# Kernel optimization log

Hardware: AMD Instinct MI355X
Metric: run time of the kernel (lower is better)

Reference implementation:

```python
import jax, jax.numpy as jnp
import numpy as np

B, N, DIM, H, DH, MLP, DEPTH = 32, 256, 384, 6, 64, 1536, 12
INNER = H * DH
LN_EPS = 1e-5
LS_INIT = 0.1  # LayerScale init_eps for depth <= 18


def setup_inputs() -> dict:
    key = jax.random.key(0)
    ks = jax.random.split(key, 10)
    f = lambda k, shape, s=0.02: jax.random.normal(k, shape, jnp.float32) * s
    return {
        "x": jax.random.normal(ks[0], (B, N, DIM), jnp.float32),
        "ln1_g": jnp.ones((DEPTH, DIM), jnp.float32),
        "ln1_b": jnp.zeros((DEPTH, DIM), jnp.float32),
        "wq": f(ks[1], (DEPTH, DIM, INNER)),
        "wkv": f(ks[2], (DEPTH, DIM, 2 * INNER)),
        "scale": jnp.full((DEPTH, H), DH ** -0.5, jnp.float32),  # learned per-head scale
        "mix_pre": f(ks[3], (DEPTH, H, H), 1.0),   # torch.randn init
        "mix_post": f(ks[4], (DEPTH, H, H), 1.0),
        "wo": f(ks[5], (DEPTH, INNER, DIM)),
        "bo": jnp.zeros((DEPTH, DIM), jnp.float32),
        "ls1": jnp.full((DEPTH, DIM), LS_INIT, jnp.float32),
        "ln2_g": jnp.ones((DEPTH, DIM), jnp.float32),
        "ln2_b": jnp.zeros((DEPTH, DIM), jnp.float32),
        "w1": f(ks[6], (DEPTH, DIM, MLP)),
        "b1": jnp.zeros((DEPTH, MLP), jnp.float32),
        "w2": f(ks[7], (DEPTH, MLP, DIM)),
        "b2": jnp.zeros((DEPTH, DIM), jnp.float32),
        "ls2": jnp.full((DEPTH, DIM), LS_INIT, jnp.float32),
    }


def _layernorm(x, g, b):
    mu = jnp.mean(x, axis=-1, keepdims=True)
    var = jnp.mean(jnp.square(x - mu), axis=-1, keepdims=True)
    return (x - mu) * jax.lax.rsqrt(var + LN_EPS) * g + b


def reference(x, ln1_g, ln1_b, wq, wkv, scale, mix_pre, mix_post, wo, bo, ls1,
              ln2_g, ln2_b, w1, b1, w2, b2, ls2):
    diag = jnp.eye(N, dtype=bool)  # self-attention diagonal mask

    def block(x, p):
        (g1, bb1, wq_, wkv_, sc, mp, mq, wo_, bo_, l1,
         g2, bb2, w1_, b1_, w2_, b2_, l2) = p
        # --- talking-heads attention (PreNorm + LayerScale + residual) ---
        y = _layernorm(x, g1, bb1)
        q = (y @ wq_).reshape(B, N, H, DH).transpose(0, 2, 1, 3)       # b h n d
        kv = y @ wkv_
        k, v = jnp.split(kv, 2, axis=-1)
        k = k.reshape(B, N, H, DH).transpose(0, 2, 1, 3)
        v = v.reshape(B, N, H, DH).transpose(0, 2, 1, 3)
        dots = jnp.einsum('bhid,bhjd->bhij', q, k) * sc[None, :, None, None]
        dots = jnp.einsum('bhij,hg->bgij', dots, mp)                   # pre-softmax head mix
        dots = jnp.where(diag, -jnp.inf, dots)                         # mask self positions
        attn = jax.nn.softmax(dots, axis=-1)
        attn = jnp.einsum('bhij,hg->bgij', attn, mq)                   # post-softmax head mix
        o = jnp.einsum('bhij,bhjd->bhid', attn, v)
        o = o.transpose(0, 2, 1, 3).reshape(B, N, INNER) @ wo_ + bo_
        x = o * l1 + x
        # --- FFN (PreNorm + LayerScale + residual) ---
        y2 = _layernorm(x, g2, bb2)
        h = jax.nn.gelu(y2 @ w1_ + b1_, approximate=False)
        x = (h @ w2_ + b2_) * l2 + x
        return x, None

    params = (ln1_g, ln1_b, wq, wkv, scale, mix_pre, mix_post, wo, bo, ls1,
              ln2_g, ln2_b, w1, b1, w2, b2, ls2)
    x, _ = jax.lax.scan(block, x, params)
    return x
```

## Files before the change

### kernel.cpp

```cpp
#include <hip/hip_runtime.h>
#include <hip/hip_bf16.h>
#include <math.h>

#define B_ 32
#define N_ 256
#define DIM_ 384
#define H_ 6
#define DH_ 64
#define INNER_ 384
#define MLP_ 1536
#define DEPTH_ 12
#define T_ (B_ * N_)

typedef __bf16 bf16x8 __attribute__((ext_vector_type(8)));
typedef __bf16 bf16x4 __attribute__((ext_vector_type(4)));
typedef float f32x4 __attribute__((ext_vector_type(4)));

typedef const __attribute__((address_space(1))) void* gas_ptr;
typedef __attribute__((address_space(3))) void* las_ptr;

#define WQKV_OFF 0
#define WO_OFF   (1152 * 384)
#define W1_OFF   (WO_OFF + 384 * 384)
#define W2_OFF   (W1_OFF + 1536 * 384)
#define WBUF_ELEMS (W2_OFF + 384 * 1536)

__global__ __launch_bounds__(256) void convert_w_all(
    const float* __restrict__ wq0, const float* __restrict__ wkv0,
    const float* __restrict__ wo0, const float* __restrict__ w10,
    const float* __restrict__ w20, __bf16* __restrict__ wbuf0)
{
    __shared__ float til[64][65];
    int t = blockIdx.x;
    int l = t / 432; t -= l * 432;
    const float* wq  = wq0  + (size_t)l * DIM_ * INNER_;
    const float* wkv = wkv0 + (size_t)l * DIM_ * 2 * INNER_;
    const float* wo  = wo0  + (size_t)l * INNER_ * DIM_;
    const float* w1  = w10  + (size_t)l * DIM_ * MLP_;
    const float* w2  = w20  + (size_t)l * MLP_ * DIM_;
    __bf16* wbuf = wbuf0 + (size_t)l * WBUF_ELEMS;

    int lane = threadIdx.x & 63, seg = threadIdx.x >> 6;
    const float* src; __bf16* dst;
    int Ns, sc, dK, dR, k0;
    if (t < 108) {
        int nt = t / 6, kt = t % 6;
        int n0 = nt * 64; k0 = kt * 64;
        dst = wbuf + WQKV_OFF; dK = 384; dR = n0;
        if (n0 < 384) { src = wq;  Ns = 384; sc = n0; }
        else          { src = wkv; Ns = 768; sc = n0 - 384; }
    } else if (t < 144) {
        int u = t - 108; int nt = u / 6, kt = u % 6;
        src = wo; Ns = 384; sc = nt * 64;
        dst = wbuf + WO_OFF; dK = 384; dR = nt * 64; k0 = kt * 64;
    } else if (t < 288) {
        int u = t - 144; int nt = u / 6, kt = u % 6;
        src = w1; Ns = 1536; sc = nt * 64;
        dst = wbuf + W1_OFF; dK = 384; dR = nt * 64; k0 = kt * 64;
    } else {
        int u = t - 288; int nt = u / 24, kt = u % 24;
        src = w2; Ns = 384; sc = nt * 64;
        dst = wbuf + W2_OFF; dK = 1536; dR = nt * 64; k0 = kt * 64;
    }
    #pragma unroll
    for (int r = 0; r < 16; ++r) {
        int i = seg * 16 + r;
        til[i][lane] = src[(size_t)(k0 + i) * Ns + sc + lane];
    }
    __syncthreads();
    #pragma unroll
    for (int r = 0; r < 16; ++r) {
        int i = seg * 16 + r;
        dst[(size_t)(dR + i) * dK + k0 + lane] = (__bf16)til[lane][i];
    }
}

__global__ __launch_bounds__(256) void ln1w(
    const float* __restrict__ x, const float* __restrict__ g,
    const float* __restrict__ b, __bf16* __restrict__ y)
{
    size_t row = blockIdx.x * 4 + (threadIdx.x >> 6);
    int lane = threadIdx.x & 63;
    const float* xr = x + row * DIM_;
    float v[6];
    #pragma unroll
    for (int s = 0; s < 6; ++s) v[s] = xr[lane + 64 * s];
    float sum = 0.f;
    #pragma unroll
    for (int s = 0; s < 6; ++s) sum += v[s];
    #pragma unroll
    for (int o = 32; o > 0; o >>= 1) sum += __shfl_xor(sum, o);
    float mu = sum * (1.0f / DIM_);
    float var = 0.f;
    #pragma unroll
    for (int s = 0; s < 6; ++s) { float d = v[s] - mu; var += d * d; }
    #pragma unroll
    for (int o = 32; o > 0; o >>= 1) var += __shfl_xor(var, o);
    float rs = rsqrtf(var * (1.0f / DIM_) + 1e-5f);
    __bf16* yr = y + row * DIM_;
    #pragma unroll
    for (int s = 0; s < 6; ++s) {
        int e = lane + 64 * s;
        yr[e] = (__bf16)((v[s] - mu) * rs * g[e] + b[e]);
    }
}

template<int MODE, int K, int BM, int BN, int BK, int NT>
__global__ __launch_bounds__(256) void gemmt(
    const __bf16* __restrict__ A, const __bf16* __restrict__ Bt,
    const float* __restrict__ bias, const float* __restrict__ ls,
    float* __restrict__ xf, __bf16* __restrict__ out,
    __bf16* __restrict__ oq, __bf16* __restrict__ ok, __bf16* __restrict__ ov,
    int Nn)
{
    constexpr int WM = BM / 32, WN = BN / 32;
    constexpr int KS = BK / 32;
    constexpr int MT = T_ / BM;
    constexpr int nIter = K / BK;
    constexpr bool SWZ = (BK == 64);
    constexpr int RPI = 512 / BK;
    constexpr int CL  = BK / 8;
    constexpr int LPT = BM / (4 * RPI) + BN / (4 * RPI);
    static_assert(LPT == 4, "vmcnt literals assume 4 loads per tile per wave");
    static_assert(nIter >= 2, "prologue stages 2 tiles");

    __shared__ __align__(16) __bf16 sA[3][BM * BK];
    __shared__ __align__(16) __bf16 sB[3][BN * BK];

    int id = blockIdx.x;
    constexpr int nxg = (MT * NT) / 8;
    int wg = (id & 7) * nxg + (id >> 3);
    int bm = (wg / NT) * BM;
    int bn = (wg % NT) * BN;
    int tid = threadIdx.x;
    int lane = tid & 63, wid = tid >> 6;
    int wm = (wid & 1) * (BM / 2), wn = (wid >> 1) * (BN / 2);
    int fm = lane & 15, fq = lane >> 4;

    f32x4 acc[WM][WN] = {};

    int lr = lane / CL, lc = lane % CL;
    int lcs = SWZ ? (lc ^ lr) : lc;
    const __bf16* aBase = A + (size_t)(bm + wid * RPI + lr) * K + lcs * 8;
    const __bf16* bBase = Bt + (size_t)(bn + wid * RPI + lr) * K + lcs * 8;

    auto stage = [&](int buf, int kk) {
        #pragma unroll
        for (int qI = 0; qI < BM / (4 * RPI); ++qI)
            __builtin_amdgcn_global_load_lds(
                (gas_ptr)(aBase + (size_t)(qI * 4 * RPI) * K + kk),
                (las_ptr)&sA[buf][qI * 2048 + wid * 512], 16, 0, 0);
        #pragma unroll
        for (int qI = 0; qI < BN / (4 * RPI); ++qI)
            __builtin_amdgcn_global_load_lds(
                (gas_ptr)(bBase + (size_t)(qI * 4 * RPI) * K + kk),
                (las_ptr)&sB[buf][qI * 2048 + wid * 512], 16, 0, 0);
    };

    stage(0, 0);
    stage(1, BK);

    #pragma unroll
    for (int i = 0; i < nIter; ++i) {
        int cur = i % 3;
        if (i + 1 < nIter)
            asm volatile("s_waitcnt vmcnt(4)" ::: "memory");
        else
            asm volatile("s_waitcnt vmcnt(0)" ::: "memory");
        __builtin_amdgcn_s_barrier();
        __builtin_amdgcn_sched_barrier(0);
        if (i + 2 < nIter)
            stage((i + 2) % 3, (i + 2) * BK);

        bf16x8 af[KS][WM], bfr[KS][WN];
        #pragma unroll
        for (int ks = 0; ks < KS; ++ks) {
            #pragma unroll
            for (int ii = 0; ii < WM; ++ii) {
                int row = wm + ii * 16 + fm;
                int c = SWZ ? (((ks * 4 + fq) ^ (row & 7)) * 8) : (ks * 32 + fq * 8);
                af[ks][ii] = *(const bf16x8*)&sA[cur][row * BK + c];
            }
            #pragma unroll
            for (int jj = 0; jj < WN; ++jj) {
                int row = wn + jj * 16 + fm;
                int c = SWZ ? (((ks * 4 + fq) ^ (row & 7)) * 8) : (ks * 32 + fq * 8);
                bfr[ks][jj] = *(const bf16x8*)&sB[cur][row * BK + c];
            }
        }
        #pragma unroll
        for (int ks = 0; ks < KS; ++ks)
            #pragma unroll
            for (int ii = 0; ii < WM; ++ii)
                #pragma unroll
                for (int jj = 0; jj < WN; ++jj)
                    acc[ii][jj] = __builtin_amdgcn_mfma_f32_16x16x32_bf16(
                        af[ks][ii], bfr[ks][jj], acc[ii][jj], 0, 0, 0);
    }

    #pragma unroll
    for (int jj = 0; jj < WN; ++jj) {
        int col = bn + wn + jj * 16 + fm;
        float bv = (MODE != 0) ? bias[col] : 0.0f;
        float lv = (MODE == 2) ? ls[col] : 0.0f;
        #pragma unroll
        for (int ii = 0; ii < WM; ++ii) {
            #pragma unroll
            for (int r = 0; r < 4; ++r) {
                int row = bm + wm + ii * 16 + fq * 4 + r;
                float v = acc[ii][jj][r];
                if (MODE == 0) {
                    if (col < 384)      oq[(size_t)row * 384 + col] = (__bf16)v;
                    else if (col < 768) ok[(size_t)row * 384 + col - 384] = (__bf16)v;
                    else {
                        int bb = row >> 8, tj = row & 255;
                        ov[((size_t)bb * 384 + (col - 768)) * 256 + tj] = (__bf16)v;
                    }
                } else if (MODE == 1) {
                    v += bv;
                    v = 0.5f * v * (1.0f + erff(v * 0.70710678118f));
                    out[(size_t)row * Nn + col] = (__bf16)v;
                } else {
                    size_t idx = (size_t)row * Nn + col;
                    xf[idx] = (v + bv) * lv + xf[idx];
                }
            }
        }
    }
}

#define PAD_S 264

__global__ __launch_bounds__(384) void attn_mfma(
    const __bf16* __restrict__ q, const __bf16* __restrict__ kb,
    const __bf16* __restrict__ vT, const float* __restrict__ scale,
    const float* __restrict__ mp, const float* __restrict__ mq,
    __bf16* __restrict__ o)
{
    __shared__ __bf16 sbuf[96][PAD_S];

    int id = blockIdx.x;
    int b = (id & 7) + ((id >> 3) & 3) * 8;
    int i0 = (id >> 5) * 16;
    int tid = threadIdx.x;
    int lane = tid & 63, wid = tid >> 6;
    int fm = lane & 15, fq = lane >> 4;

    int h = wid;
    bf16x8 qf[2];
    #pragma unroll
    for (int ks = 0; ks < 2; ++ks)
        qf[ks] = *(const bf16x8*)&q[(size_t)(b * 256 + i0 + fm) * 384 + h * 64 + ks * 32 + fq * 8];
    #pragma unroll 4
    for (int jt = 0; jt < 16; ++jt) {
        f32x4 a = {};
        #pragma unroll
        for (int ks = 0; ks < 2; ++ks) {
            bf16x8 bfr = *(const bf16x8*)&kb[(size_t)(b * 256 + jt * 16 + fm) * 384 + h * 64 + ks * 32 + fq * 8];
            a = __builtin_amdgcn_mfma_f32_16x16x32_bf16(qf[ks], bfr, a, 0, 0, 0);
        }
        #pragma unroll
        for (int r = 0; r < 4; ++r)
            sbuf[h * 16 + fq * 4 + r][jt * 16 + fm] = (__bf16)a[r];
    }

    float mps[36], mqs[36];
    #pragma unroll
    for (int t = 0; t < 36; ++t) { mps[t] = mp[t] * scale[t / 6]; mqs[t] = mq[t]; }

    __syncthreads();

    for (int i = wid; i < 16; i += 6) {
        float sv[6][4];
        #pragma unroll
        for (int h2 = 0; h2 < 6; ++h2) {
            bf16x4 v4 = *(const bf16x4*)&sbuf[h2 * 16 + i][lane * 4];
            #pragma unroll
            for (int c = 0; c < 4; ++c) sv[h2][c] = (float)v4[c];
        }
        int drow = i0 + i;
        float pv[6][4];
        #pragma unroll
        for (int g2 = 0; g2 < 6; ++g2) {
            float t0[4];
            #pragma unroll
            for (int c = 0; c < 4; ++c) {
                float r2 = 0.f;
                #pragma unroll
                for (int h2 = 0; h2 < 6; ++h2) r2 += sv[h2][c] * mps[h2 * 6 + g2];
                t0[c] = (lane * 4 + c == drow) ? -1e30f : r2;
            }
            float m = fmaxf(fmaxf(t0[0], t0[1]), fmaxf(t0[2], t0[3]));
            #pragma unroll
            for (int off = 32; off > 0; off >>= 1) m = fmaxf(m, __shfl_xor(m, off));
            float e0 = __expf(t0[0] - m), e1 = __expf(t0[1] - m);
            float e2 = __expf(t0[2] - m), e3 = __expf(t0[3] - m);
            float s = e0 + e1 + e2 + e3;
            #pragma unroll
            for (int off = 32; off > 0; off >>= 1) s += __shfl_xor(s, off);
            float inv = 1.0f / s;
            pv[g2][0] = e0 * inv; pv[g2][1] = e1 * inv;
            pv[g2][2] = e2 * inv; pv[g2][3] = e3 * inv;
        }
        #pragma unroll
        for (int g2 = 0; g2 < 6; ++g2) {
            bf16x4 w4;
            #pragma unroll
            for (int c = 0; c < 4; ++c) {
                float r2 = 0.f;
                #pragma unroll
                for (int h2 = 0; h2 < 6; ++h2) r2 += pv[h2][c] * mqs[h2 * 6 + g2];
                w4[c] = (__bf16)r2;
            }
            *(bf16x4*)&sbuf[g2 * 16 + i][lane * 4] = w4;
        }
    }
    __syncthreads();

    int gg = wid;
    f32x4 acco[4] = {};
    #pragma unroll
    for (int jc = 0; jc < 4; ++jc) {
        #pragma unroll
        for (int ks = 0; ks < 2; ++ks) {
            bf16x8 af = *(const bf16x8*)&sbuf[gg * 16 + fm][jc * 64 + ks * 32 + fq * 8];
            #pragma unroll
            for (int nt = 0; nt < 4; ++nt) {
                bf16x8 bfr = *(const bf16x8*)&vT[(size_t)(b * 384 + gg * 64 + nt * 16 + fm) * 256 + jc * 64 + ks * 32 + fq * 8];
                acco[nt] = __builtin_amdgcn_mfma_f32_16x16x32_bf16(af, bfr, acco[nt], 0, 0, 0);
            }
        }
    }
    #pragma unroll
    for (int nt = 0; nt < 4; ++nt)
        #pragma unroll
        for (int r = 0; r < 4; ++r)
            o[(size_t)(b * 256 + i0 + fq * 4 + r) * 384 + gg * 64 + nt * 16 + fm] = (__bf16)acco[nt][r];
}

extern "C" void kernel_launch(void* const* d_in, const int* in_sizes, int n_in,
                              void* d_out, int out_size, void* d_ws, size_t ws_size,
                              hipStream_t stream) {
    const float* x      = (const float*)d_in[0];
    const float* ln1_g  = (const float*)d_in[1];
    const float* ln1_b  = (const float*)d_in[2];
    const float* wq     = (const float*)d_in[3];
    const float* wkv    = (const float*)d_in[4];
    const float* scale  = (const float*)d_in[5];
    const float* mixp   = (const float*)d_in[6];
    const float* mixq   = (const float*)d_in[7];
    const float* wo     = (const float*)d_in[8];
    const float* bo     = (const float*)d_in[9];
    const float* ls1    = (const float*)d_in[10];
    const float* ln2_g  = (const float*)d_in[11];
    const float* ln2_b  = (const float*)d_in[12];
    const float* w1     = (const float*)d_in[13];
    const float* b1     = (const float*)d_in[14];
    const float* w2     = (const float*)d_in[15];
    const float* b2     = (const float*)d_in[16];
    const float* ls2    = (const float*)d_in[17];

    char* ws = (char*)d_ws;
    float*  xf = (float*)ws;                      ws += (size_t)T_ * DIM_ * 4;
    __bf16* y  = (__bf16*)ws;                     ws += (size_t)T_ * DIM_ * 2;
    __bf16* q  = (__bf16*)ws;                     ws += (size_t)T_ * DIM_ * 2;
    __bf16* kb = (__bf16*)ws;                     ws += (size_t)T_ * DIM_ * 2;
    __bf16* vT = (__bf16*)ws;                     ws += (size_t)T_ * DIM_ * 2;
    __bf16* o  = (__bf16*)ws;                     ws += (size_t)T_ * DIM_ * 2;
    __bf16* wbuf = (__bf16*)ws;                   ws += (size_t)WBUF_ELEMS * DEPTH_ * 2;
    __bf16* h  = q;

    size_t nBytes = (size_t)T_ * DIM_ * sizeof(float);
    hipMemcpyAsync(xf, x, nBytes, hipMemcpyDeviceToDevice, stream);

    convert_w_all<<<432 * DEPTH_, 256, 0, stream>>>(wq, wkv, wo, w1, w2, wbuf);

    for (int l = 0; l < DEPTH_; ++l) {
        __bf16* wl = wbuf + (size_t)l * WBUF_ELEMS;

        ln1w<<<T_ / 4, 256, 0, stream>>>(xf, ln1_g + (size_t)l * DIM_, ln1_b + (size_t)l * DIM_, y);

        gemmt<0, 384, 128, 128, 32, 9><<<576, 256, 0, stream>>>(
            y, wl + WQKV_OFF, nullptr, nullptr, nullptr, nullptr,
            q, kb, vT, 1152);

        attn_mfma<<<512, 384, 0, stream>>>(
            q, kb, vT, scale + (size_t)l * H_,
            mixp + (size_t)l * H_ * H_, mixq + (size_t)l * H_ * H_, o);

        gemmt<2, 384, 64, 64, 64, 6><<<768, 256, 0, stream>>>(
            o, wl + WO_OFF, bo + (size_t)l * DIM_, ls1 + (size_t)l * DIM_,
            xf, nullptr, nullptr, nullptr, nullptr, DIM_);

        ln1w<<<T_ / 4, 256, 0, stream>>>(xf, ln2_g + (size_t)l * DIM_, ln2_b + (size_t)l * DIM_, y);

        gemmt<1, 384, 128, 128, 32, 12><<<768, 256, 0, stream>>>(
            y, wl + W1_OFF, b1 + (size_t)l * MLP_, nullptr,
            nullptr, h, nullptr, nullptr, nullptr, MLP_);

        gemmt<2, 1536, 64, 64, 64, 6><<<768, 256, 0, stream>>>(
            h, wl + W2_OFF, b2 + (size_t)l * DIM_, ls2 + (size_t)l * DIM_,
            xf, nullptr, nullptr, nullptr, nullptr, DIM_);
    }

    hipMemcpyAsync(d_out, xf, nBytes, hipMemcpyDeviceToDevice, stream);
}
```

Measured before the change: 1.643 ms.

## Fuse LayerNorm into GEMM A-loading with residual-epilogue row statistics

Removes the two per-layer LayerNorm kernels. The residual GEMM epilogues now accumulate per-row sum and sum of squares with atomics. The QKV and FFN1 GEMMs read the fp32 residual directly, normalize it on the fly from those stats, and write bf16 into shared memory in place of the async global-to-LDS A loads. This saves two launches and a bf16 intermediate round trip per layer. In exchange it adds atomics, a register-staged A path, and a variance computed as E[x²]−mu², which is less numerically stable than the two-pass form.

```diff
diff --git a/kernel.cpp b/kernel.cpp
--- a/kernel.cpp
+++ b/kernel.cpp
@@ -75,43 +75,30 @@
     }
 }
 
-__global__ __launch_bounds__(256) void ln1w(
-    const float* __restrict__ x, const float* __restrict__ g,
-    const float* __restrict__ b, __bf16* __restrict__ y)
+__global__ __launch_bounds__(256) void row_stats(
+    const float* __restrict__ x, float* __restrict__ st)
 {
     size_t row = blockIdx.x * 4 + (threadIdx.x >> 6);
     int lane = threadIdx.x & 63;
     const float* xr = x + row * DIM_;
-    float v[6];
-    #pragma unroll
-    for (int s = 0; s < 6; ++s) v[s] = xr[lane + 64 * s];
-    float sum = 0.f;
-    #pragma unroll
-    for (int s = 0; s < 6; ++s) sum += v[s];
-    #pragma unroll
-    for (int o = 32; o > 0; o >>= 1) sum += __shfl_xor(sum, o);
-    float mu = sum * (1.0f / DIM_);
-    float var = 0.f;
-    #pragma unroll
-    for (int s = 0; s < 6; ++s) { float d = v[s] - mu; var += d * d; }
-    #pragma unroll
-    for (int o = 32; o > 0; o >>= 1) var += __shfl_xor(var, o);
-    float rs = rsqrtf(var * (1.0f / DIM_) + 1e-5f);
-    __bf16* yr = y + row * DIM_;
-    #pragma unroll
-    for (int s = 0; s < 6; ++s) {
-        int e = lane + 64 * s;
-        yr[e] = (__bf16)((v[s] - mu) * rs * g[e] + b[e]);
-    }
+    float s = 0.f, q2 = 0.f;
+    #pragma unroll
+    for (int k = 0; k < 6; ++k) { float v = xr[lane + 64 * k]; s += v; q2 += v * v; }
+    #pragma unroll
+    for (int o = 32; o > 0; o >>= 1) { s += __shfl_xor(s, o); q2 += __shfl_xor(q2, o); }
+    if (lane == 0) { st[row * 2] = s; st[row * 2 + 1] = q2; }
 }
 
-template<int MODE, int K, int BM, int BN, int BK, int NT>
+template<int MODE, int K, int BM, int BN, int BK, int NT, bool LNA>
 __global__ __launch_bounds__(256) void gemmt(
     const __bf16* __restrict__ A, const __bf16* __restrict__ Bt,
     const float* __restrict__ bias, const float* __restrict__ ls,
     float* __restrict__ xf, __bf16* __restrict__ out,
     __bf16* __restrict__ oq, __bf16* __restrict__ ok, __bf16* __restrict__ ov,
-    int Nn)
+    int Nn,
+    const float* __restrict__ xin, const float* __restrict__ stats,
+    const float* __restrict__ lng, const float* __restrict__ lnb,
+    float* __restrict__ statsOut, float* __restrict__ statsZero)
 {
     constexpr int WM = BM / 32, WN = BN / 32;
     constexpr int KS = BK / 32;
@@ -120,12 +107,12 @@
     constexpr bool SWZ = (BK == 64);
     constexpr int RPI = 512 / BK;
     constexpr int CL  = BK / 8;
-    constexpr int LPT = BM / (4 * RPI) + BN / (4 * RPI);
-    static_assert(LPT == 4, "vmcnt literals assume 4 loads per tile per wave");
-    static_assert(nIter >= 2, "prologue stages 2 tiles");
+    static_assert(!LNA || (BM == 128 && BK == 32 && K == 384), "LNA mapping");
+    static_assert(nIter >= 3, "pipeline needs >=3 K-steps");
 
     __shared__ __align__(16) __bf16 sA[3][BM * BK];
     __shared__ __align__(16) __bf16 sB[3][BN * BK];
+    __shared__ float sLN[LNA ? 768 : 4];
 
     int id = blockIdx.x;
     constexpr int nxg = (MT * NT) / 8;
@@ -137,19 +124,16 @@
     int wm = (wid & 1) * (BM / 2), wn = (wid >> 1) * (BN / 2);
     int fm = lane & 15, fq = lane >> 4;
 
+    if (statsZero != nullptr && (wg % NT) == 0 && tid < 2 * BM)
+        statsZero[(size_t)bm * 2 + tid] = 0.f;
+
     f32x4 acc[WM][WN] = {};
 
     int lr = lane / CL, lc = lane % CL;
     int lcs = SWZ ? (lc ^ lr) : lc;
-    const __bf16* aBase = A + (size_t)(bm + wid * RPI + lr) * K + lcs * 8;
     const __bf16* bBase = Bt + (size_t)(bn + wid * RPI + lr) * K + lcs * 8;
 
-    auto stage = [&](int buf, int kk) {
-        #pragma unroll
-        for (int qI = 0; qI < BM / (4 * RPI); ++qI)
-            __builtin_amdgcn_global_load_lds(
-                (gas_ptr)(aBase + (size_t)(qI * 4 * RPI) * K + kk),
-                (las_ptr)&sA[buf][qI * 2048 + wid * 512], 16, 0, 0);
+    auto stageB = [&](int buf, int kk) {
         #pragma unroll
         for (int qI = 0; qI < BN / (4 * RPI); ++qI)
             __builtin_amdgcn_global_load_lds(
@@ -157,21 +141,7 @@
                 (las_ptr)&sB[buf][qI * 2048 + wid * 512], 16, 0, 0);
     };
 
-    stage(0, 0);
-    stage(1, BK);
-
-    #pragma unroll
-    for (int i = 0; i < nIter; ++i) {
-        int cur = i % 3;
-        if (i + 1 < nIter)
-            asm volatile("s_waitcnt vmcnt(4)" ::: "memory");
-        else
-            asm volatile("s_waitcnt vmcnt(0)" ::: "memory");
-        __builtin_amdgcn_s_barrier();
-        __builtin_amdgcn_sched_barrier(0);
-        if (i + 2 < nIter)
-            stage((i + 2) % 3, (i + 2) * BK);
-
+    auto compute = [&](int cur) {
         bf16x8 af[KS][WM], bfr[KS][WN];
         #pragma unroll
         for (int ks = 0; ks < KS; ++ks) {
@@ -196,8 +166,96 @@
                 for (int jj = 0; jj < WN; ++jj)
                     acc[ii][jj] = __builtin_amdgcn_mfma_f32_16x16x32_bf16(
                         af[ks][ii], bfr[ks][jj], acc[ii][jj], 0, 0, 0);
-    }
-
+    };
+
+    if constexpr (LNA) {
+        int r0 = wid * 32 + lr, r1 = r0 + 16;
+        for (int t2 = tid; t2 < 384; t2 += 256) { sLN[t2] = lng[t2]; sLN[384 + t2] = lnb[t2]; }
+        __syncthreads();
+
+        float2 st0 = *(const float2*)&stats[(size_t)(bm + r0) * 2];
+        float2 st1 = *(const float2*)&stats[(size_t)(bm + r1) * 2];
+        float mu0 = st0.x * (1.f / 384.f), mu1 = st1.x * (1.f / 384.f);
+        float rs0 = rsqrtf(st0.y * (1.f / 384.f) - mu0 * mu0 + 1e-5f);
+        float rs1 = rsqrtf(st1.y * (1.f / 384.f) - mu1 * mu1 + 1e-5f);
+        __builtin_amdgcn_sched_barrier(0);
+
+        f32x4 ar[2][2][2];
+        const float* xr0 = xin + (size_t)(bm + r0) * 384 + lc * 8;
+        const float* xr1 = xin + (size_t)(bm + r1) * 384 + lc * 8;
+        auto loadA = [&](int set, int t) {
+            ar[set][0][0] = *(const f32x4*)(xr0 + t * 32);
+            ar[set][0][1] = *(const f32x4*)(xr0 + t * 32 + 4);
+            ar[set][1][0] = *(const f32x4*)(xr1 + t * 32);
+            ar[set][1][1] = *(const f32x4*)(xr1 + t * 32 + 4);
+        };
+        auto writeA = [&](int set, int buf, int t) {
+            f32x4 gv0 = *(const f32x4*)&sLN[t * 32 + lc * 8];
+            f32x4 gv1 = *(const f32x4*)&sLN[t * 32 + lc * 8 + 4];
+            f32x4 bv0 = *(const f32x4*)&sLN[384 + t * 32 + lc * 8];
+            f32x4 bv1 = *(const f32x4*)&sLN[384 + t * 32 + lc * 8 + 4];
+            bf16x8 w0, w1;
+            #pragma unroll
+            for (int k2 = 0; k2 < 4; ++k2) {
+                w0[k2]     = (__bf16)((ar[set][0][0][k2] - mu0) * rs0 * gv0[k2] + bv0[k2]);
+                w0[k2 + 4] = (__bf16)((ar[set][0][1][k2] - mu0) * rs0 * gv1[k2] + bv1[k2]);
+                w1[k2]     = (__bf16)((ar[set][1][0][k2] - mu1) * rs1 * gv0[k2] + bv0[k2]);
+                w1[k2 + 4] = (__bf16)((ar[set][1][1][k2] - mu1) * rs1 * gv1[k2] + bv1[k2]);
+            }
+            *(bf16x8*)&sA[buf][r0 * 32 + lc * 8] = w0;
+            *(bf16x8*)&sA[buf][r1 * 32 + lc * 8] = w1;
+        };
+
+        loadA(0, 0); stageB(0, 0);
+        loadA(1, 1); stageB(1, BK);
+        writeA(0, 0, 0);
+
+        #pragma unroll
+        for (int i = 0; i < nIter; ++i) {
+            int cur = i % 3;
+            if (i + 1 < nIter) asm volatile("s_waitcnt vmcnt(6)" ::: "memory");
+            else               asm volatile("s_waitcnt vmcnt(0)" ::: "memory");
+            asm volatile("s_waitcnt lgkmcnt(0)" ::: "memory");
+            __builtin_amdgcn_sched_barrier(0);
+            __builtin_amdgcn_s_barrier();
+            __builtin_amdgcn_sched_barrier(0);
+            if (i + 2 < nIter) { loadA(i % 2, i + 2); stageB((i + 2) % 3, (i + 2) * BK); }
+            if (i + 1 < nIter) writeA((i + 1) % 2, (i + 1) % 3, i + 1);
+            compute(cur);
+        }
+    } else {
+        const __bf16* aBase = A + (size_t)(bm + wid * RPI + lr) * K + lcs * 8;
+        auto stageA = [&](int buf, int kk) {
+            #pragma unroll
+            for (int qI = 0; qI < BM / (4 * RPI); ++qI)
+                __builtin_amdgcn_global_load_lds(
+                    (gas_ptr)(aBase + (size_t)(qI * 4 * RPI) * K + kk),
+                    (las_ptr)&sA[buf][qI * 2048 + wid * 512], 16, 0, 0);
+        };
+        stageA(0, 0); stageB(0, 0);
+        stageA(1, BK); stageB(1, BK);
+
+        #pragma unroll
+        for (int i = 0; i < nIter; ++i) {
+            int cur = i % 3;
+            if (i + 1 < nIter)
+                asm volatile("s_waitcnt vmcnt(4)" ::: "memory");
+            else
+                asm volatile("s_waitcnt vmcnt(0)" ::: "memory");
+            __builtin_amdgcn_s_barrier();
+            __builtin_amdgcn_sched_barrier(0);
+            if (i + 2 < nIter) { stageA((i + 2) % 3, (i + 2) * BK); stageB((i + 2) % 3, (i + 2) * BK); }
+            compute(cur);
+        }
+    }
+
+    float sS[WM][4], sQ[WM][4];
+    if constexpr (MODE == 2) {
+        #pragma unroll
+        for (int ii = 0; ii < WM; ++ii)
+            #pragma unroll
+            for (int r = 0; r < 4; ++r) { sS[ii][r] = 0.f; sQ[ii][r] = 0.f; }
+    }
     #pragma unroll
     for (int jj = 0; jj < WN; ++jj) {
         int col = bn + wn + jj * 16 + fm;
@@ -222,7 +280,27 @@
                     out[(size_t)row * Nn + col] = (__bf16)v;
                 } else {
                     size_t idx = (size_t)row * Nn + col;
-                    xf[idx] = (v + bv) * lv + xf[idx];
+                    float nv = (v + bv) * lv + xf[idx];
+                    xf[idx] = nv;
+                    sS[ii][r] += nv; sQ[ii][r] += nv * nv;
+                }
+            }
+        }
+    }
+    if constexpr (MODE == 2) {
+        if (statsOut != nullptr) {
+            #pragma unroll
+            for (int ii = 0; ii < WM; ++ii) {
+                #pragma unroll
+                for (int r = 0; r < 4; ++r) {
+                    float a = sS[ii][r], b = sQ[ii][r];
+                    #pragma unroll
+                    for (int o = 8; o > 0; o >>= 1) { a += __shfl_xor(a, o); b += __shfl_xor(b, o); }
+                    if (fm == 0) {
+                        int row = bm + wm + ii * 16 + fq * 4 + r;
+                        atomicAdd(&statsOut[(size_t)row * 2], a);
+                        atomicAdd(&statsOut[(size_t)row * 2 + 1], b);
+                    }
                 }
             }
         }
@@ -362,7 +440,9 @@
 
     char* ws = (char*)d_ws;
     float*  xf = (float*)ws;                      ws += (size_t)T_ * DIM_ * 4;
-    __bf16* y  = (__bf16*)ws;                     ws += (size_t)T_ * DIM_ * 2;
+    float*  statsLn1 = (float*)ws;
+    float*  statsLn2 = statsLn1 + 2 * T_;
+    ws += (size_t)T_ * DIM_ * 2;
     __bf16* q  = (__bf16*)ws;                     ws += (size_t)T_ * DIM_ * 2;
     __bf16* kb = (__bf16*)ws;                     ws += (size_t)T_ * DIM_ * 2;
     __bf16* vT = (__bf16*)ws;                     ws += (size_t)T_ * DIM_ * 2;
@@ -374,33 +454,36 @@
     hipMemcpyAsync(xf, x, nBytes, hipMemcpyDeviceToDevice, stream);
 
     convert_w_all<<<432 * DEPTH_, 256, 0, stream>>>(wq, wkv, wo, w1, w2, wbuf);
+    row_stats<<<T_ / 4, 256, 0, stream>>>(xf, statsLn1);
 
     for (int l = 0; l < DEPTH_; ++l) {
         __bf16* wl = wbuf + (size_t)l * WBUF_ELEMS;
 
-        ln1w<<<T_ / 4, 256, 0, stream>>>(xf, ln1_g + (size_t)l * DIM_, ln1_b + (size_t)l * DIM_, y);
-
-        gemmt<0, 384, 128, 128, 32, 9><<<576, 256, 0, stream>>>(
-            y, wl + WQKV_OFF, nullptr, nullptr, nullptr, nullptr,
-            q, kb, vT, 1152);
+        gemmt<0, 384, 128, 128, 32, 9, true><<<576, 256, 0, stream>>>(
+            nullptr, wl + WQKV_OFF, nullptr, nullptr, nullptr, nullptr,
+            q, kb, vT, 1152,
+            xf, statsLn1, ln1_g + (size_t)l * DIM_, ln1_b + (size_t)l * DIM_,
+            nullptr, statsLn2);
 
         attn_mfma<<<512, 384, 0, stream>>>(
             q, kb, vT, scale + (size_t)l * H_,
             mixp + (size_t)l * H_ * H_, mixq + (size_t)l * H_ * H_, o);
 
-        gemmt<2, 384, 64, 64, 64, 6><<<768, 256, 0, stream>>>(
+        gemmt<2, 384, 64, 64, 64, 6, false><<<768, 256, 0, stream>>>(
             o, wl + WO_OFF, bo + (size_t)l * DIM_, ls1 + (size_t)l * DIM_,
-            xf, nullptr, nullptr, nullptr, nullptr, DIM_);
-
-        ln1w<<<T_ / 4, 256, 0, stream>>>(xf, ln2_g + (size_t)l * DIM_, ln2_b + (size_t)l * DIM_, y);
-
-        gemmt<1, 384, 128, 128, 32, 12><<<768, 256, 0, stream>>>(
-            y, wl + W1_OFF, b1 + (size_t)l * MLP_, nullptr,
-            nullptr, h, nullptr, nullptr, nullptr, MLP_);
-
-        gemmt<2, 1536, 64, 64, 64, 6><<<768, 256, 0, stream>>>(
+            xf, nullptr, nullptr, nullptr, nullptr, DIM_,
+            nullptr, nullptr, nullptr, nullptr, statsLn2, statsLn1);
+
+        gemmt<1, 384, 128, 128, 32, 12, true><<<768, 256, 0, stream>>>(
+            nullptr, wl + W1_OFF, b1 + (size_t)l * MLP_, nullptr,
+            nullptr, h, nullptr, nullptr, nullptr, MLP_,
+            xf, statsLn2, ln2_g + (size_t)l * DIM_, ln2_b + (size_t)l * DIM_,
+            nullptr, nullptr);
+
+        gemmt<2, 1536, 64, 64, 64, 6, false><<<768, 256, 0, stream>>>(
             h, wl + W2_OFF, b2 + (size_t)l * DIM_, ls2 + (size_t)l * DIM_,
-            xf, nullptr, nullptr, nullptr, nullptr, DIM_);
+            xf, nullptr, nullptr, nullptr, nullptr, DIM_,
+            nullptr, nullptr, nullptr, nullptr, statsLn1, nullptr);
     }
 
     hipMemcpyAsync(d_out, xf, nBytes, hipMemcpyDeviceToDevice, stream);
```

Measured after the change: 1.886 ms. 14.8% more time.
